# Kernel tuning notes

Measured on AMD Instinct MI355X. Metric: run time of the kernel, lower is better.

## Reference

```python
import jax, jax.numpy as jnp
import numpy as np

HEAD_DIM = 4  # hard-coded by rosa_4bit_layer's reshape(B, T, -1, 4)


def setup_inputs() -> dict:
    key = jax.random.key(0)
    B, T, C = 4, 4096, 512
    kq, kk, kv = jax.random.split(key, 3)
    xq = jax.random.normal(kq, (B, T, C), dtype=jnp.float32)
    xk = jax.random.normal(kk, (B, T, C), dtype=jnp.float32)
    xv = jax.random.normal(kv, (B, T, C), dtype=jnp.float32)
    emb = jnp.ones((1, 1, C), dtype=jnp.float32)  # nn.Parameter(torch.ones((1,1,C)))
    return {"xq": xq, "xk": xk, "xv": xv, "emb": emb}


def _rosa_sufa(q, k, v):
    # q,k,v: (B, H, T, d) with d = 4.
    # Causal linear-attention recurrence with per-head d x d state:
    #   S_t = S_{t-1} + k_t v_t^T ;  o_t = q_t^T S_t
    # expressed as a cumulative sum over outer products (vectorized over T).
    kv = jnp.cumsum(k[..., :, None] * v[..., None, :], axis=2)  # (B,H,T,d,d)
    return jnp.einsum('bhtd,bhtde->bhte', q, kv)                # (B,H,T,d)


def reference(xq, xk, xv, emb):
    B, T, C = xq.shape
    H = C // HEAD_DIM
    # (B,T,C) -> (B,T,H,4) -> (B,H,T,4)
    q = xq.reshape(B, T, H, HEAD_DIM).transpose(0, 2, 1, 3)
    k = xk.reshape(B, T, H, HEAD_DIM).transpose(0, 2, 1, 3)
    v = xv.reshape(B, T, H, HEAD_DIM).transpose(0, 2, 1, 3)
    o = _rosa_sufa(q, k, v)
    # (B,H,T,4) -> (B,T,C)
    o = o.transpose(0, 2, 1, 3).reshape(B, T, C)
    return o * emb
```

## Files before the change

kernel.cpp:

```cpp
#include <hip/hip_runtime.h>


constexpr int B  = 4;
constexpr int T  = 4096;
constexpr int C  = 512;
constexpr int CT = 32;
constexpr int NC = T / CT;

__global__ __launch_bounds__(512) void rosa_partial(const float* __restrict__ k,
                                                    const float* __restrict__ v,
                                                    float* __restrict__ part) {
  const int bc  = blockIdx.x;
  const int b   = bc / NC;
  const int c   = bc % NC;
  const int tid = threadIdx.x;
  const int h   = tid >> 2;
  const int e   = tid & 3;

  const size_t base = ((size_t)b * T + (size_t)c * CT) * (size_t)C + (h << 2);
  const float* kb = k + base;
  const float* vb = v + base + e;

  float4 acc = {0.f, 0.f, 0.f, 0.f};
#pragma unroll 8
  for (int t = 0; t < CT; ++t) {
    const float4 k4 = *reinterpret_cast<const float4*>(kb + (size_t)t * C);
    const float  ve = vb[(size_t)t * C];
    acc.x += k4.x * ve;
    acc.y += k4.y * ve;
    acc.z += k4.z * ve;
    acc.w += k4.w * ve;
  }
  reinterpret_cast<float4*>(part)[(size_t)bc * 512 + tid] = acc;
}

__global__ __launch_bounds__(512) void rosa_scan_out(const float* __restrict__ q,
                                                     const float* __restrict__ k,
                                                     const float* __restrict__ v,
                                                     const float* __restrict__ emb,
                                                     const float* __restrict__ part,
                                                     float* __restrict__ out) {
  const int bc  = blockIdx.x;
  const int b   = bc / NC;
  const int c   = bc % NC;
  const int tid = threadIdx.x;
  const int h   = tid >> 2;
  const int e   = tid & 3;

  float4 S = {0.f, 0.f, 0.f, 0.f};
  const float4* pb = reinterpret_cast<const float4*>(part) + (size_t)b * NC * 512 + tid;
#pragma unroll 4
  for (int cp = 0; cp < c; ++cp) {
    const float4 p4 = pb[(size_t)cp * 512];
    S.x += p4.x;
    S.y += p4.y;
    S.z += p4.z;
    S.w += p4.w;
  }

  const size_t base = ((size_t)b * T + (size_t)c * CT) * (size_t)C + (h << 2);
  const float* qb = q + base;
  const float* kb = k + base;
  const float* vb = v + base + e;
  float*       ob = out + base + e;
  const float embv = emb[(h << 2) + e];

#pragma unroll 8
  for (int t = 0; t < CT; ++t) {
    const float4 k4 = *reinterpret_cast<const float4*>(kb + (size_t)t * C);
    const float4 q4 = *reinterpret_cast<const float4*>(qb + (size_t)t * C);
    const float  ve = vb[(size_t)t * C];
    S.x += k4.x * ve;
    S.y += k4.y * ve;
    S.z += k4.z * ve;
    S.w += k4.w * ve;
    const float o = q4.x * S.x + q4.y * S.y + q4.z * S.z + q4.w * S.w;
    ob[(size_t)t * C] = o * embv;
  }
}

extern "C" void kernel_launch(void* const* d_in, const int* in_sizes, int n_in,
                              void* d_out, int out_size, void* d_ws, size_t ws_size,
                              hipStream_t stream) {
  const float* xq  = (const float*)d_in[0];
  const float* xk  = (const float*)d_in[1];
  const float* xv  = (const float*)d_in[2];
  const float* emb = (const float*)d_in[3];
  float* out  = (float*)d_out;
  float* part = (float*)d_ws;

  rosa_partial<<<B * NC, 512, 0, stream>>>(xk, xv, part);
  rosa_scan_out<<<B * NC, 512, 0, stream>>>(xq, xk, xv, emb, part, out);
}
```

Before: 164.1 us.

## Add two-level hierarchical prefix over chunk partials to shorten scan loop

Adds a kernel that sums each group of 16 chunk partial states into super-chunk partials. The scan/output kernel then reads at most 7 super-partials plus up to 15 chunk partials instead of up to 127 chunk partials per block. This cuts the quadratic prefix-read traffic and the serial dependent loads at the cost of an extra kernel launch and a small extra workspace region.

```diff
diff --git a/kernel.cpp b/kernel.cpp
--- a/kernel.cpp
+++ b/kernel.cpp
@@ -1,11 +1,14 @@
 #include <hip/hip_runtime.h>
 
 
-constexpr int B  = 4;
-constexpr int T  = 4096;
-constexpr int C  = 512;
-constexpr int CT = 32;
-constexpr int NC = T / CT;
+constexpr int B   = 4;
+constexpr int T   = 4096;
+constexpr int C   = 512;
+constexpr int CT  = 32;
+constexpr int NC  = T / CT;
+constexpr int SC  = 16;
+constexpr int NSC = NC / SC;
+constexpr size_t SPART_OFF = (size_t)B * NC * 2048;
 
 __global__ __launch_bounds__(512) void rosa_partial(const float* __restrict__ k,
                                                     const float* __restrict__ v,
@@ -34,11 +37,35 @@
   reinterpret_cast<float4*>(part)[(size_t)bc * 512 + tid] = acc;
 }
 
+__global__ __launch_bounds__(128) void rosa_super(const float* __restrict__ part,
+                                                  float* __restrict__ spart) {
+  const int blk = blockIdx.x;
+  const int g   = blk & 3;
+  const int bs  = blk >> 2;
+  const int b   = bs / NSC;
+  const int s   = bs % NSC;
+  const int j   = (g << 7) + threadIdx.x;
+
+  const float4* p4 = reinterpret_cast<const float4*>(part) +
+                     ((size_t)(b * NC + s * SC)) * 512 + j;
+  float4 acc = {0.f, 0.f, 0.f, 0.f};
+#pragma unroll
+  for (int i = 0; i < SC; ++i) {
+    const float4 v4 = p4[(size_t)i * 512];
+    acc.x += v4.x;
+    acc.y += v4.y;
+    acc.z += v4.z;
+    acc.w += v4.w;
+  }
+  reinterpret_cast<float4*>(spart)[(size_t)bs * 512 + j] = acc;
+}
+
 __global__ __launch_bounds__(512) void rosa_scan_out(const float* __restrict__ q,
                                                      const float* __restrict__ k,
                                                      const float* __restrict__ v,
                                                      const float* __restrict__ emb,
                                                      const float* __restrict__ part,
+                                                     const float* __restrict__ spart,
                                                      float* __restrict__ out) {
   const int bc  = blockIdx.x;
   const int b   = bc / NC;
@@ -46,16 +73,22 @@
   const int tid = threadIdx.x;
   const int h   = tid >> 2;
   const int e   = tid & 3;
+  const int s   = c >> 4;
+  const int cr  = c & (SC - 1);
 
   float4 S = {0.f, 0.f, 0.f, 0.f};
-  const float4* pb = reinterpret_cast<const float4*>(part) + (size_t)b * NC * 512 + tid;
+  const float4* sp = reinterpret_cast<const float4*>(spart) + (size_t)b * NSC * 512 + tid;
 #pragma unroll 4
-  for (int cp = 0; cp < c; ++cp) {
-    const float4 p4 = pb[(size_t)cp * 512];
-    S.x += p4.x;
-    S.y += p4.y;
-    S.z += p4.z;
-    S.w += p4.w;
+  for (int i = 0; i < s; ++i) {
+    const float4 p4 = sp[(size_t)i * 512];
+    S.x += p4.x; S.y += p4.y; S.z += p4.z; S.w += p4.w;
+  }
+  const float4* pb = reinterpret_cast<const float4*>(part) +
+                     ((size_t)(b * NC + s * SC)) * 512 + tid;
+#pragma unroll 4
+  for (int i = 0; i < cr; ++i) {
+    const float4 p4 = pb[(size_t)i * 512];
+    S.x += p4.x; S.y += p4.y; S.z += p4.z; S.w += p4.w;
   }
 
   const size_t base = ((size_t)b * T + (size_t)c * CT) * (size_t)C + (h << 2);
@@ -86,9 +119,11 @@
   const float* xk  = (const float*)d_in[1];
   const float* xv  = (const float*)d_in[2];
   const float* emb = (const float*)d_in[3];
-  float* out  = (float*)d_out;
-  float* part = (float*)d_ws;
+  float* out   = (float*)d_out;
+  float* part  = (float*)d_ws;
+  float* spart = part + SPART_OFF;
 
   rosa_partial<<<B * NC, 512, 0, stream>>>(xk, xv, part);
-  rosa_scan_out<<<B * NC, 512, 0, stream>>>(xq, xk, xv, emb, part, out);
+  rosa_super<<<B * NSC * 4, 128, 0, stream>>>(part, spart);
+  rosa_scan_out<<<B * NC, 512, 0, stream>>>(xq, xk, xv, emb, part, spart, out);
 }
```

Result: faster. 151.3 us (-7.8%).
